# Kernel tuning notes

Hardware: AMD Instinct MI355X
Metric: run time of the kernel (lower is better)

The kernel has to match this reference:

```python
import jax, jax.numpy as jnp
import numpy as np

B, NX, NY = 16, 1024, 1024
DIN_X, DIN_Y = 768, 283
DK, DV, NH = 80, 80, 8
HK, HV = DK // NH, DV // NH  # 10, 10
NORM = 1.0 / np.sqrt(HK)


def setup_inputs() -> dict:
    key = jax.random.key(0)
    kx, ky, kq, kk, kv = jax.random.split(key, 5)
    x = jax.random.normal(kx, (B, NX, DIN_X), dtype=jnp.float32)
    y = jax.random.normal(ky, (B, NY, DIN_Y), dtype=jnp.float32)
    attn_mask = jnp.zeros((B, NX, NY), dtype=jnp.float32)  # unused in forward (dead arg in original)
    # torch nn.Linear weights are [out, in]; kaiming-uniform-ish init scale
    Wq = jax.random.normal(kq, (DK, DIN_X), dtype=jnp.float32) / np.sqrt(DIN_X)
    Wk = jax.random.normal(kk, (DK, DIN_Y), dtype=jnp.float32) / np.sqrt(DIN_Y)
    Wv = jax.random.normal(kv, (DV, DIN_Y), dtype=jnp.float32) / np.sqrt(DIN_Y)
    return {"x": x, "y": y, "attn_mask": attn_mask, "Wq": Wq, "Wk": Wk, "Wv": Wv}


def reference(x, y, attn_mask, Wq, Wk, Wv):
    b, n_x, _ = x.shape
    n_y = y.shape[1]
    # projections (Linear, no bias): [B,N,D] @ W^T
    q = (x @ Wq.T).reshape(b, n_x, NH, HK).transpose(0, 2, 1, 3)  # [B,H,Nx,hk]
    k = (y @ Wk.T).reshape(b, n_y, NH, HK).transpose(0, 2, 1, 3)  # [B,H,Ny,hk]
    v = (y @ Wv.T).reshape(b, n_y, NH, HV).transpose(0, 2, 1, 3)  # [B,H,Ny,hv]
    scores = jnp.einsum("bhqd,bhkd->bhqk", q, k) * NORM          # [B,H,Nx,Ny]
    dist = jax.nn.softmax(scores, axis=-1)
    # dropout p=0.5 is identity in eval mode
    att = jnp.einsum("bhqk,bhkd->bhqd", dist, v)                  # [B,H,Nx,hv]
    att = att.transpose(0, 2, 1, 3).reshape(b, n_x, DV)           # [B,Nx,dim_v]
    return att, dist
```

## Files before the change

### kernel.cpp

```cpp
#include <hip/hip_runtime.h>
#include <hip/hip_bf16.h>

#define BB 16
#define NXX 1024
#define NYY 1024
#define DINX 768
#define DINY 283
#define NHH 8
#define HKK 10
#define DKV 80
#define NORMF 0.31622776601683794f

#define NPLANE (BB * NXX * DKV)
#define SLD 1032


__global__ __launch_bounds__(256) void proj_q(
    const float* __restrict__ X, const float* __restrict__ Wq, float* __restrict__ Pq) {
  __shared__ float Xs[64 * 33];
  const int t = threadIdx.x;
  const int rt = blockIdx.x >> 2;
  const int ks = blockIdx.x & 3;
  const int w = __builtin_amdgcn_readfirstlane(t >> 6);
  const int lane = t & 63;
  const int cbase = w * 20;
  const int kbase = ks * 192;

  float acc[20];
#pragma unroll
  for (int c = 0; c < 20; ++c) acc[c] = 0.f;

#pragma unroll 1
  for (int ch = 0; ch < 6; ++ch) {
    const int dk = kbase + ch * 32;
    __syncthreads();
    for (int u = t; u < 2048; u += 256) {
      const int r = u >> 5, c = u & 31;
      Xs[r * 33 + c] = X[(size_t)(rt * 64 + r) * DINX + dk + c];
    }
    __syncthreads();
    float xv[32];
#pragma unroll
    for (int k = 0; k < 32; ++k) xv[k] = Xs[lane * 33 + k];
#pragma unroll
    for (int c = 0; c < 20; ++c) {
      const float* wr = Wq + (size_t)(cbase + c) * DINX + dk;
#pragma unroll
      for (int k = 0; k < 32; ++k) acc[c] = fmaf(wr[k], xv[k], acc[c]);
    }
  }

  const int row = rt * 64 + lane;
  const int b = row >> 10, n = row & 1023;
  float* dst = Pq + (size_t)ks * NPLANE;
#pragma unroll
  for (int c = 0; c < 20; ++c) {
    const int cc = cbase + c, h = cc / 10, d = cc - 10 * h;
    dst[(((size_t)b * NHH + h) * 1024 + n) * 10 + d] = acc[c];
  }
}

__global__ __launch_bounds__(512) void proj_kv(
    const float* __restrict__ Y, const float* __restrict__ WK, const float* __restrict__ WV,
    float* __restrict__ Pk, float* __restrict__ Pv) {
  __shared__ float Xs[64 * 33];
  const int t = threadIdx.x;
  const int rt = blockIdx.x >> 1;
  const int ks = blockIdx.x & 1;
  const int w = __builtin_amdgcn_readfirstlane(t >> 6);
  const int lane = t & 63;
  const bool isV = (w >= 4);
  const int cbase = (isV ? (w - 4) : w) * 20;
  const float* W = isV ? WV : WK;
  const int kbase = ks * 160;
  const int nch = ks ? 4 : 5;

  float acc[20];
#pragma unroll
  for (int c = 0; c < 20; ++c) acc[c] = 0.f;

#pragma unroll 1
  for (int ch = 0; ch < nch; ++ch) {
    const int dk = kbase + ch * 32;
    __syncthreads();
    for (int u = t; u < 2048; u += 512) {
      const int r = u >> 5, c = u & 31;
      const int d = dk + c;
      Xs[r * 33 + c] = (d < DINY) ? Y[(size_t)(rt * 64 + r) * DINY + d] : 0.f;
    }
    __syncthreads();
    float xv[32];
#pragma unroll
    for (int k = 0; k < 32; ++k) xv[k] = Xs[lane * 33 + k];
    if (dk + 32 <= DINY) {
#pragma unroll
      for (int c = 0; c < 20; ++c) {
        const float* wr = W + (size_t)(cbase + c) * DINY + dk;
#pragma unroll
        for (int k = 0; k < 32; ++k) acc[c] = fmaf(wr[k], xv[k], acc[c]);
      }
    } else {
#pragma unroll
      for (int c = 0; c < 20; ++c) {
        const float* wr = W + (size_t)(cbase + c) * DINY + dk;
#pragma unroll
        for (int k = 0; k < 27; ++k) acc[c] = fmaf(wr[k], xv[k], acc[c]);
      }
    }
  }

  const int row = rt * 64 + lane;
  const int b = row >> 10, n = row & 1023;
  float* dst = (isV ? Pv : Pk) + (size_t)ks * NPLANE;
#pragma unroll
  for (int c = 0; c < 20; ++c) {
    const int cc = cbase + c, h = cc / 10, d = cc - 10 * h;
    dst[(((size_t)b * NHH + h) * 10 + d) * 1024 + n] = acc[c];
  }
}

__global__ __launch_bounds__(256) void reduce_k(const float* __restrict__ ws, float* __restrict__ F) {
  const int NI = NPLANE / 4;
  const float4* Pq = (const float4*)ws;
  const float4* Pk = (const float4*)(ws + (size_t)4 * NPLANE);
  const float4* Pv = (const float4*)(ws + (size_t)6 * NPLANE);
  float4* Fo = (float4*)F;
  for (int i = blockIdx.x * 256 + threadIdx.x; i < 3 * NI; i += gridDim.x * 256) {
    float4 s;
    if (i < NI) {
      float4 a = Pq[i], b2 = Pq[i + NI], c = Pq[i + 2 * NI], d = Pq[i + 3 * NI];
      s.x = a.x + b2.x + c.x + d.x; s.y = a.y + b2.y + c.y + d.y;
      s.z = a.z + b2.z + c.z + d.z; s.w = a.w + b2.w + c.w + d.w;
    } else if (i < 2 * NI) {
      const int j = i - NI;
      float4 a = Pk[j], b2 = Pk[j + NI];
      s.x = a.x + b2.x; s.y = a.y + b2.y; s.z = a.z + b2.z; s.w = a.w + b2.w;
    } else {
      const int j = i - 2 * NI;
      float4 a = Pv[j], b2 = Pv[j + NI];
      s.x = a.x + b2.x; s.y = a.y + b2.y; s.z = a.z + b2.z; s.w = a.w + b2.w;
    }
    Fo[i] = s;
  }
}

__global__ __launch_bounds__(512, 2) void attn_kernel(
    const float* __restrict__ Qhm, const float* __restrict__ Kdm,
    const float* __restrict__ Vdm, float* __restrict__ out_att,
    float* __restrict__ out_dist) {
  __shared__ __hip_bfloat16 S[32 * SLD];
  __shared__ float rls[32];

  const int t = threadIdx.x;
  const int bid = blockIdx.x;
  const int qt = bid & 31;
  const int h = (bid >> 5) & 7;
  const int b = bid >> 8;

  const int w = __builtin_amdgcn_readfirstlane(t >> 6);
  const int kl = t & 63;

  float qr[4][10];
#pragma unroll
  for (int qi = 0; qi < 4; ++qi) {
    const float2* qp = (const float2*)(Qhm + (((size_t)b * NHH + h) * 1024 + qt * 32 + w * 4 + qi) * 10);
#pragma unroll
    for (int dd = 0; dd < 5; ++dd) {
      float2 v = qp[dd];
      qr[qi][2 * dd] = v.x * NORMF;
      qr[qi][2 * dd + 1] = v.y * NORMF;
    }
  }

  const float* kp = Kdm + (size_t)(b * NHH + h) * 10 * 1024;
  const float* vp = Vdm + (size_t)(b * NHH + h) * 10 * 1024;

  float acc[4][10];
#pragma unroll
  for (int qi = 0; qi < 4; ++qi)
#pragma unroll
    for (int d = 0; d < 10; ++d) acc[qi][d] = 0.f;
  float lsum[4] = {0.f, 0.f, 0.f, 0.f};

#pragma unroll 2
  for (int j = 0; j < 16; ++j) {
    const int k = j * 64 + kl;
    float kf[10];
#pragma unroll
    for (int d = 0; d < 10; ++d) kf[d] = kp[d * 1024 + k];
    float p[4];
#pragma unroll
    for (int qi = 0; qi < 4; ++qi) {
      float s = qr[qi][0] * kf[0] + qr[qi][1] * kf[1] + qr[qi][2] * kf[2] +
                qr[qi][3] * kf[3] + qr[qi][4] * kf[4] + qr[qi][5] * kf[5] +
                qr[qi][6] * kf[6] + qr[qi][7] * kf[7] + qr[qi][8] * kf[8] +
                qr[qi][9] * kf[9];
      p[qi] = __expf(s);
      lsum[qi] += p[qi];
      S[(w * 4 + qi) * SLD + k] = __float2bfloat16(p[qi]);
    }
    float vf[10];
#pragma unroll
    for (int d = 0; d < 10; ++d) vf[d] = vp[d * 1024 + k];
#pragma unroll
    for (int qi = 0; qi < 4; ++qi)
#pragma unroll
      for (int d = 0; d < 10; ++d) acc[qi][d] += p[qi] * vf[d];
  }

#pragma unroll
  for (int off = 32; off; off >>= 1) {
#pragma unroll
    for (int qi = 0; qi < 4; ++qi) {
      lsum[qi] += __shfl_xor(lsum[qi], off);
#pragma unroll
      for (int d = 0; d < 10; ++d) acc[qi][d] += __shfl_xor(acc[qi][d], off);
    }
  }

  if (kl == 0) {
#pragma unroll
    for (int qi = 0; qi < 4; ++qi) {
      const int q = w * 4 + qi;
      const float rl = 1.0f / lsum[qi];
      rls[q] = rl;
      float* ap = out_att + ((size_t)b * NXX + qt * 32 + q) * DKV + h * HKK;
#pragma unroll
      for (int dd = 0; dd < 5; ++dd)
        *(float2*)&ap[2 * dd] = make_float2(acc[qi][2 * dd] * rl, acc[qi][2 * dd + 1] * rl);
    }
  }
  __syncthreads();

  const size_t dbase = (((size_t)(b * NHH + h)) * NXX + qt * 32) * NYY;
#pragma unroll 2
  for (int it = 0; it < 16; ++it) {
    const int e = it * 2048 + (t << 2);
    const int qq = e >> 10;
    const int kk = e & 1023;
    uint2 wv = *(const uint2*)&S[qq * SLD + kk];
    const float rlq = rls[qq];
    float4 o;
    o.x = __uint_as_float(wv.x << 16) * rlq;
    o.y = __uint_as_float(wv.x & 0xffff0000u) * rlq;
    o.z = __uint_as_float(wv.y << 16) * rlq;
    o.w = __uint_as_float(wv.y & 0xffff0000u) * rlq;
    *(float4*)(out_dist + dbase + (size_t)qq * NYY + kk) = o;
  }
}

extern "C" void kernel_launch(void* const* d_in, const int* in_sizes, int n_in,
                              void* d_out, int out_size, void* d_ws, size_t ws_size,
                              hipStream_t stream) {
  (void)in_sizes; (void)n_in; (void)out_size; (void)ws_size;
  const float* x = (const float*)d_in[0];
  const float* y = (const float*)d_in[1];
  const float* Wq = (const float*)d_in[3];
  const float* Wk = (const float*)d_in[4];
  const float* Wv = (const float*)d_in[5];

  float* out = (float*)d_out;
  float* att_out = out;
  float* dist_out = out + (size_t)BB * NXX * DKV;

  float* ws = (float*)d_ws;
  float* Pq = ws;
  float* Pk = ws + (size_t)4 * NPLANE;
  float* Pv = ws + (size_t)6 * NPLANE;
  float* F  = ws + (size_t)8 * NPLANE;
  float* Qhm = F;
  float* Kdm = F + (size_t)NPLANE;
  float* Vdm = F + (size_t)2 * NPLANE;

  proj_q<<<1024, 256, 0, stream>>>(x, Wq, Pq);
  proj_kv<<<512, 512, 0, stream>>>(y, Wk, Wv, Pk, Pv);
  reduce_k<<<2048, 256, 0, stream>>>(ws, F);
  attn_kernel<<<BB * NHH * 32, 512, 0, stream>>>(Qhm, Kdm, Vdm, att_out, dist_out);
}
```

Measured before the change: 563.8 us.

## Recompute softmax probabilities for dist instead of staging bf16 scores in LDS

The attention kernel now runs one query per lane in 64-thread blocks. Each lane streams interleaved K/V records, a 32-float row layout written by the K/V projection, to get the row sum and the attention output. A second pass then recomputes exp(q·k) per pair, scaled by the reciprocal sum, writing fp32 dist directly instead of rounding through bf16 shared memory. NORM is folded into K at projection time, and the K/V layout is changed to pair-interleaved and padded-record forms. This trades doubled exp/dot work and a larger KV workspace for better accuracy and less shared memory, but the tiny blocks and the uniform per-lane loads of the same K/V record may limit throughput.

```diff
diff --git a/kernel.cpp b/kernel.cpp
--- a/kernel.cpp
+++ b/kernel.cpp
@@ -11,9 +11,16 @@
 #define DKV 80
 #define NORMF 0.31622776601683794f
 
-#define NPLANE (BB * NXX * DKV)
-#define SLD 1032
-
+#define NP 1310720UL
+#define NR2 4194304UL
+
+
+__device__ __forceinline__ float dot10(const float* a, const float* b) {
+  float s = a[0] * b[0];
+#pragma unroll
+  for (int d = 1; d < 10; ++d) s = fmaf(a[d], b[d], s);
+  return s;
+}
 
 __global__ __launch_bounds__(256) void proj_q(
     const float* __restrict__ X, const float* __restrict__ Wq, float* __restrict__ Pq) {
@@ -52,7 +59,7 @@
 
   const int row = rt * 64 + lane;
   const int b = row >> 10, n = row & 1023;
-  float* dst = Pq + (size_t)ks * NPLANE;
+  float* dst = Pq + (size_t)ks * NP;
 #pragma unroll
   for (int c = 0; c < 20; ++c) {
     const int cc = cbase + c, h = cc / 10, d = cc - 10 * h;
@@ -62,7 +69,7 @@
 
 __global__ __launch_bounds__(512) void proj_kv(
     const float* __restrict__ Y, const float* __restrict__ WK, const float* __restrict__ WV,
-    float* __restrict__ Pk, float* __restrict__ Pv) {
+    float* __restrict__ PKd, float* __restrict__ PKr) {
   __shared__ float Xs[64 * 33];
   const int t = threadIdx.x;
   const int rt = blockIdx.x >> 1;
@@ -111,141 +118,128 @@
 
   const int row = rt * 64 + lane;
   const int b = row >> 10, n = row & 1023;
-  float* dst = (isV ? Pv : Pk) + (size_t)ks * NPLANE;
 #pragma unroll
   for (int c = 0; c < 20; ++c) {
     const int cc = cbase + c, h = cc / 10, d = cc - 10 * h;
-    dst[(((size_t)b * NHH + h) * 10 + d) * 1024 + n] = acc[c];
+    const size_t bh = (size_t)b * NHH + h;
+    const size_t grow = bh * 1024 + n;
+    if (!isV) {
+      const float v = acc[c] * NORMF;
+      PKd[(size_t)ks * NP + (bh * 5 + (d >> 1)) * 2048 + n * 2 + (d & 1)] = v;
+      PKr[(size_t)ks * NR2 + grow * 32 + d] = v;
+    } else {
+      PKr[(size_t)ks * NR2 + grow * 32 + 16 + d] = acc[c];
+    }
   }
 }
 
 __global__ __launch_bounds__(256) void reduce_k(const float* __restrict__ ws, float* __restrict__ F) {
-  const int NI = NPLANE / 4;
-  const float4* Pq = (const float4*)ws;
-  const float4* Pk = (const float4*)(ws + (size_t)4 * NPLANE);
-  const float4* Pv = (const float4*)(ws + (size_t)6 * NPLANE);
-  float4* Fo = (float4*)F;
-  for (int i = blockIdx.x * 256 + threadIdx.x; i < 3 * NI; i += gridDim.x * 256) {
+  const int NIQ = NP / 4;
+  const int NIK = NP / 4;
+  const int NIR = NR2 / 4;
+  const float4* w4 = (const float4*)ws;
+  float4* F4 = (float4*)F;
+  const int total = NIQ + NIK + NIR;
+  for (int i = blockIdx.x * 256 + threadIdx.x; i < total; i += gridDim.x * 256) {
     float4 s;
-    if (i < NI) {
-      float4 a = Pq[i], b2 = Pq[i + NI], c = Pq[i + 2 * NI], d = Pq[i + 3 * NI];
-      s.x = a.x + b2.x + c.x + d.x; s.y = a.y + b2.y + c.y + d.y;
-      s.z = a.z + b2.z + c.z + d.z; s.w = a.w + b2.w + c.w + d.w;
-    } else if (i < 2 * NI) {
-      const int j = i - NI;
-      float4 a = Pk[j], b2 = Pk[j + NI];
-      s.x = a.x + b2.x; s.y = a.y + b2.y; s.z = a.z + b2.z; s.w = a.w + b2.w;
+    if (i < NIQ) {
+      const float4* P = w4;
+      float4 a = P[i], b = P[i + NIQ], c = P[i + 2 * NIQ], d = P[i + 3 * NIQ];
+      s.x = a.x + b.x + c.x + d.x; s.y = a.y + b.y + c.y + d.y;
+      s.z = a.z + b.z + c.z + d.z; s.w = a.w + b.w + c.w + d.w;
+      F4[i] = s;
+    } else if (i < NIQ + NIK) {
+      const int j = i - NIQ;
+      const float4* P = w4 + 4 * NIQ;
+      float4 a = P[j], b = P[j + NIK];
+      s.x = a.x + b.x; s.y = a.y + b.y; s.z = a.z + b.z; s.w = a.w + b.w;
+      F4[i] = s;
     } else {
-      const int j = i - 2 * NI;
-      float4 a = Pv[j], b2 = Pv[j + NI];
-      s.x = a.x + b2.x; s.y = a.y + b2.y; s.z = a.z + b2.z; s.w = a.w + b2.w;
-    }
-    Fo[i] = s;
-  }
-}
-
-__global__ __launch_bounds__(512, 2) void attn_kernel(
+      const int j = i - NIQ - NIK;
+      const float4* P = w4 + 6 * NIQ;
+      float4 a = P[j], b = P[j + NIR];
+      s.x = a.x + b.x; s.y = a.y + b.y; s.z = a.z + b.z; s.w = a.w + b.w;
+      F4[i] = s;
+    }
+  }
+}
+
+__global__ __launch_bounds__(64) void attn_kernel(
     const float* __restrict__ Qhm, const float* __restrict__ Kdm,
-    const float* __restrict__ Vdm, float* __restrict__ out_att,
+    const float* __restrict__ KVr, float* __restrict__ out_att,
     float* __restrict__ out_dist) {
-  __shared__ __hip_bfloat16 S[32 * SLD];
-  __shared__ float rls[32];
-
-  const int t = threadIdx.x;
+  __shared__ float qs[64 * 12];
+
+  const int lane = threadIdx.x;
   const int bid = blockIdx.x;
-  const int qt = bid & 31;
-  const int h = (bid >> 5) & 7;
-  const int b = bid >> 8;
-
-  const int w = __builtin_amdgcn_readfirstlane(t >> 6);
-  const int kl = t & 63;
-
-  float qr[4][10];
-#pragma unroll
-  for (int qi = 0; qi < 4; ++qi) {
-    const float2* qp = (const float2*)(Qhm + (((size_t)b * NHH + h) * 1024 + qt * 32 + w * 4 + qi) * 10);
+  const int nt = bid & 15;
+  const int bh = bid >> 4;
+  const int n = nt * 64 + lane;
+
+  float qr[10];
+  {
+    const float2* qp = (const float2*)(Qhm + ((size_t)bh * 1024 + n) * 10);
 #pragma unroll
     for (int dd = 0; dd < 5; ++dd) {
       float2 v = qp[dd];
-      qr[qi][2 * dd] = v.x * NORMF;
-      qr[qi][2 * dd + 1] = v.y * NORMF;
-    }
-  }
-
-  const float* kp = Kdm + (size_t)(b * NHH + h) * 10 * 1024;
-  const float* vp = Vdm + (size_t)(b * NHH + h) * 10 * 1024;
-
-  float acc[4][10];
-#pragma unroll
-  for (int qi = 0; qi < 4; ++qi)
-#pragma unroll
-    for (int d = 0; d < 10; ++d) acc[qi][d] = 0.f;
-  float lsum[4] = {0.f, 0.f, 0.f, 0.f};
-
+      qr[2 * dd] = v.x; qr[2 * dd + 1] = v.y;
+    }
+  }
+
+  float acc[10];
+#pragma unroll
+  for (int d = 0; d < 10; ++d) acc[d] = 0.f;
+  float l = 0.f;
+
+  const float4* kv4 = (const float4*)(KVr + (size_t)bh * 1024 * 32);
 #pragma unroll 2
-  for (int j = 0; j < 16; ++j) {
-    const int k = j * 64 + kl;
-    float kf[10];
-#pragma unroll
-    for (int d = 0; d < 10; ++d) kf[d] = kp[d * 1024 + k];
-    float p[4];
-#pragma unroll
-    for (int qi = 0; qi < 4; ++qi) {
-      float s = qr[qi][0] * kf[0] + qr[qi][1] * kf[1] + qr[qi][2] * kf[2] +
-                qr[qi][3] * kf[3] + qr[qi][4] * kf[4] + qr[qi][5] * kf[5] +
-                qr[qi][6] * kf[6] + qr[qi][7] * kf[7] + qr[qi][8] * kf[8] +
-                qr[qi][9] * kf[9];
-      p[qi] = __expf(s);
-      lsum[qi] += p[qi];
-      S[(w * 4 + qi) * SLD + k] = __float2bfloat16(p[qi]);
-    }
-    float vf[10];
-#pragma unroll
-    for (int d = 0; d < 10; ++d) vf[d] = vp[d * 1024 + k];
-#pragma unroll
-    for (int qi = 0; qi < 4; ++qi)
-#pragma unroll
-      for (int d = 0; d < 10; ++d) acc[qi][d] += p[qi] * vf[d];
-  }
-
-#pragma unroll
-  for (int off = 32; off; off >>= 1) {
-#pragma unroll
-    for (int qi = 0; qi < 4; ++qi) {
-      lsum[qi] += __shfl_xor(lsum[qi], off);
-#pragma unroll
-      for (int d = 0; d < 10; ++d) acc[qi][d] += __shfl_xor(acc[qi][d], off);
-    }
-  }
-
-  if (kl == 0) {
-#pragma unroll
-    for (int qi = 0; qi < 4; ++qi) {
-      const int q = w * 4 + qi;
-      const float rl = 1.0f / lsum[qi];
-      rls[q] = rl;
-      float* ap = out_att + ((size_t)b * NXX + qt * 32 + q) * DKV + h * HKK;
-#pragma unroll
-      for (int dd = 0; dd < 5; ++dd)
-        *(float2*)&ap[2 * dd] = make_float2(acc[qi][2 * dd] * rl, acc[qi][2 * dd + 1] * rl);
-    }
-  }
+  for (int k = 0; k < 1024; ++k) {
+    const float4* rec = kv4 + (size_t)k * 8;
+    float4 a0 = rec[0], a1 = rec[1], a2 = rec[2];
+    float kf[10] = {a0.x, a0.y, a0.z, a0.w, a1.x, a1.y, a1.z, a1.w, a2.x, a2.y};
+    const float p = __expf(dot10(qr, kf));
+    l += p;
+    float4 b0 = rec[4], b1 = rec[5], b2 = rec[6];
+    float vf[10] = {b0.x, b0.y, b0.z, b0.w, b1.x, b1.y, b1.z, b1.w, b2.x, b2.y};
+#pragma unroll
+    for (int d = 0; d < 10; ++d) acc[d] = fmaf(p, vf[d], acc[d]);
+  }
+
+  const float rl = 1.0f / l;
+  {
+    float* ap = out_att + ((size_t)(bh >> 3) * 1024 + n) * DKV + (bh & 7) * HKK;
+#pragma unroll
+    for (int dd = 0; dd < 5; ++dd)
+      *(float2*)&ap[2 * dd] = make_float2(acc[2 * dd] * rl, acc[2 * dd + 1] * rl);
+  }
+#pragma unroll
+  for (int d = 0; d < 10; ++d) qs[lane * 12 + d] = qr[d];
+  qs[lane * 12 + 10] = rl;
   __syncthreads();
 
-  const size_t dbase = (((size_t)(b * NHH + h)) * NXX + qt * 32) * NYY;
-#pragma unroll 2
-  for (int it = 0; it < 16; ++it) {
-    const int e = it * 2048 + (t << 2);
-    const int qq = e >> 10;
-    const int kk = e & 1023;
-    uint2 wv = *(const uint2*)&S[qq * SLD + kk];
-    const float rlq = rls[qq];
-    float4 o;
-    o.x = __uint_as_float(wv.x << 16) * rlq;
-    o.y = __uint_as_float(wv.x & 0xffff0000u) * rlq;
-    o.z = __uint_as_float(wv.y << 16) * rlq;
-    o.w = __uint_as_float(wv.y & 0xffff0000u) * rlq;
-    *(float4*)(out_dist + dbase + (size_t)qq * NYY + kk) = o;
+  const float4* kp4 = (const float4*)(Kdm + (size_t)bh * 10240);
+  float* drow = out_dist + ((size_t)bh * 1024 + (size_t)nt * 64) * 1024;
+#pragma unroll 1
+  for (int c = 0; c < 8; ++c) {
+    const int kb = c * 128 + lane * 2;
+    float kA[10], kB[10];
+#pragma unroll
+    for (int dp = 0; dp < 5; ++dp) {
+      float4 v = kp4[dp * 512 + (kb >> 1)];
+      kA[2 * dp] = v.x; kA[2 * dp + 1] = v.y;
+      kB[2 * dp] = v.z; kB[2 * dp + 1] = v.w;
+    }
+#pragma unroll 4
+    for (int qq = 0; qq < 64; ++qq) {
+      float4 qa = *(const float4*)&qs[qq * 12];
+      float4 qb = *(const float4*)&qs[qq * 12 + 4];
+      float4 qc = *(const float4*)&qs[qq * 12 + 8];
+      float qv[10] = {qa.x, qa.y, qa.z, qa.w, qb.x, qb.y, qb.z, qb.w, qc.x, qc.y};
+      const float rlq = qc.z;
+      const float p0 = __expf(dot10(qv, kA)) * rlq;
+      const float p1 = __expf(dot10(qv, kB)) * rlq;
+      *(float2*)&drow[(size_t)qq * 1024 + kb] = make_float2(p0, p1);
+    }
   }
 }
 
@@ -264,16 +258,16 @@
   float* dist_out = out + (size_t)BB * NXX * DKV;
 
   float* ws = (float*)d_ws;
-  float* Pq = ws;
-  float* Pk = ws + (size_t)4 * NPLANE;
-  float* Pv = ws + (size_t)6 * NPLANE;
-  float* F  = ws + (size_t)8 * NPLANE;
+  float* Pq  = ws;
+  float* PKd = ws + 4 * NP;
+  float* PKr = ws + 6 * NP;
+  float* F   = ws + 8 * NP + 2 * NR2;
   float* Qhm = F;
-  float* Kdm = F + (size_t)NPLANE;
-  float* Vdm = F + (size_t)2 * NPLANE;
+  float* Kdm = F + NP;
+  float* KVr = F + 2 * NP;
 
   proj_q<<<1024, 256, 0, stream>>>(x, Wq, Pq);
-  proj_kv<<<512, 512, 0, stream>>>(y, Wk, Wv, Pk, Pv);
+  proj_kv<<<512, 512, 0, stream>>>(y, Wk, Wv, PKd, PKr);
   reduce_k<<<2048, 256, 0, stream>>>(ws, F);
-  attn_kernel<<<BB * NHH * 32, 512, 0, stream>>>(Qhm, Kdm, Vdm, att_out, dist_out);
-}
+  attn_kernel<<<BB * NHH * 16, 64, 0, stream>>>(Qhm, Kdm, KVr, att_out, dist_out);
+}
```

Result: faster. 543.5 us (-3.6%).
